# Kernel optimization log

Hardware: AMD Instinct MI355X
Metric: run time of the kernel (lower is better)

Reference implementation:

```python
import jax, jax.numpy as jnp
import numpy as np

EPS = 1e-5


def conv1d(x, w, b):
    # x: (B, C_in, S), w: (C_out, C_in, K), 'same' padding = K//2
    pad = w.shape[-1] // 2
    y = jax.lax.conv_general_dilated(
        x, w, window_strides=(1,), padding=[(pad, pad)],
        dimension_numbers=("NCH", "OIH", "NCH"))
    return y + b[None, :, None]


def layer_norm(x, g, b):
    m = jnp.mean(x, axis=-1, keepdims=True)
    v = jnp.var(x, axis=-1, keepdims=True)
    return (x - m) * jax.lax.rsqrt(v + EPS) * g + b


def duration_predict(x, conv1_w, conv1_b, conv2_w, conv2_b,
                     ln1_g, ln1_b, ln2_g, ln2_b, lin_w, lin_b):
    # x: (B, S, C)
    out = conv1d(jnp.swapaxes(x, -2, -1), conv1_w, conv1_b)          # (B, F, S)
    out = jax.nn.relu(layer_norm(jnp.swapaxes(out, -2, -1), ln1_g, ln1_b))  # (B, S, F)
    out = conv1d(jnp.swapaxes(out, -2, -1), conv2_w, conv2_b)        # (B, F, S)
    out = jax.nn.relu(layer_norm(jnp.swapaxes(out, -2, -1), ln2_g, ln2_b))  # (B, S, F)
    out = jax.nn.relu(out @ lin_w.T + lin_b)                          # (B, S, 1)
    return jnp.squeeze(out, -1)                                       # (B, S)


def setup_inputs() -> dict:
    key = jax.random.key(0)
    ks = jax.random.split(key, 6)
    B, S, C = 16, 1024, 256
    F_, K = 256, 3
    inp = {
        "x": jax.random.normal(ks[0], (B, S, C), dtype=jnp.float32),
        "target": jax.random.uniform(ks[1], (B, S), dtype=jnp.float32),
        "conv1_w": jax.random.normal(ks[2], (F_, C, K), dtype=jnp.float32) * 0.02,
        "conv1_b": jnp.zeros((F_,), dtype=jnp.float32),
        "conv2_w": jax.random.normal(ks[3], (F_, F_, K), dtype=jnp.float32) * 0.02,
        "conv2_b": jnp.zeros((F_,), dtype=jnp.float32),
        "ln1_g": jnp.ones((F_,), dtype=jnp.float32),
        "ln1_b": jnp.zeros((F_,), dtype=jnp.float32),
        "ln2_g": jnp.ones((F_,), dtype=jnp.float32),
        "ln2_b": jnp.zeros((F_,), dtype=jnp.float32),
        "lin_w": jax.random.normal(ks[4], (1, F_), dtype=jnp.float32) * 0.02,
        "lin_b": jnp.zeros((1,), dtype=jnp.float32),
    }
    return inp


def reference(x, target, conv1_w, conv1_b, conv2_w, conv2_b,
              ln1_g, ln1_b, ln2_g, ln2_b, lin_w, lin_b):
    reg_len = duration_predict(x, conv1_w, conv1_b, conv2_w, conv2_b,
                               ln1_g, ln1_b, ln2_g, ln2_b, lin_w, lin_b)
    # Faithful to the original: max_len uses exp(target), the mask uses round(target).
    # max_len is data-dependent -> computed from concrete target (host-side, like the original).
    max_len = int(np.round(float(jnp.max(jnp.sum(jnp.exp(target), axis=-1)))))
    d = jnp.round(target)                 # (B, S) integer-valued durations (banker's rounding, like Python round)
    fin = jnp.cumsum(d, axis=-1)          # (B, S) end offsets
    start = fin - d                       # (B, S) start offsets
    t = jnp.arange(max_len, dtype=target.dtype)  # (T,)
    mask = ((t[None, None, :] >= start[..., None]) &
            (t[None, None, :] < fin[..., None])).astype(x.dtype)  # (B, S, T)
    # x.transpose @ mask -> (B, C, T) -> transpose -> (B, T, C)
    expanded = jnp.einsum("bsc,bst->btc", x, mask)
    return expanded, reg_len
```

## Files before the change

kernel.cpp:

```cpp
#include <hip/hip_runtime.h>
#include <hip/hip_bf16.h>

using frag_ab = __attribute__((ext_vector_type(8))) short;
using frag_cd = __attribute__((ext_vector_type(4))) float;

#define SLEN 1024
#define CDIM 256
#define KTOT 768
#define PD 8

static __device__ __forceinline__ short f2bf(float f) {
    __hip_bfloat16 h = __float2bfloat16(f);
    return *reinterpret_cast<short*>(&h);
}

__global__ __launch_bounds__(1024) void scan_repack_kernel(
    const float* __restrict__ target, int* __restrict__ src, int T,
    const float* __restrict__ w1, __hip_bfloat16* __restrict__ bt1,
    const float* __restrict__ w2, __hip_bfloat16* __restrict__ bt2)
{
    __shared__ int waveSum[16];
    const int tid = threadIdx.x;

    if (blockIdx.x < 16) {
        const int b = blockIdx.x;
        for (int i = tid; i < T; i += 1024) src[b * T + i] = -1;

        const float tv = target[b * SLEN + tid];
        const int d = (int)rintf(tv);

        const int lane = tid & 63;
        const int wid = tid >> 6;
        int v = d;
#pragma unroll
        for (int off = 1; off < 64; off <<= 1) {
            int n = __shfl_up(v, off);
            if (lane >= off) v += n;
        }
        if (lane == 63) waveSum[wid] = v;
        __syncthreads();
        if (tid < 16) {
            int wv = waveSum[tid];
#pragma unroll
            for (int off = 1; off < 16; off <<= 1) {
                int n = __shfl_up(wv, off);
                if (tid >= off) wv += n;
            }
            waveSum[tid] = wv;
        }
        __syncthreads();
        const int fin = v + (wid > 0 ? waveSum[wid - 1] : 0);
        const int start = fin - d;
        for (int t = start; t < fin; ++t)
            if (t >= 0 && t < T) src[b * T + t] = tid;
    } else {
        const int id = (blockIdx.x - 16) * 1024 + tid;
        const int which = id >= 196608;
        const int e = which ? id - 196608 : id;
        const int f = e / KTOT;
        const int K = e - f * KTOT;
        const int k3 = K >> 8;
        const int c = K & 255;
        const float* w = which ? w2 : w1;
        __hip_bfloat16* bt = which ? bt2 : bt1;
        bt[f * KTOT + K] = __float2bfloat16(w[f * KTOT + c * 3 + k3]);
    }
}

__global__ __launch_bounds__(256) void expand_kernel(
    const float* __restrict__ x, const int* __restrict__ src,
    float* __restrict__ out, int T)
{
    const int row = blockIdx.x * 4 + (threadIdx.x >> 6);
    const int lane = threadIdx.x & 63;
    const int nrows = 16 * T;
    if (row >= nrows) return;
    const int b = row / T;
    const int s = src[row];
    float4 val = make_float4(0.f, 0.f, 0.f, 0.f);
    if (s >= 0)
        val = *(const float4*)(x + ((size_t)(b * SLEN + s)) * CDIM + lane * 4);
    *(float4*)(out + (size_t)row * CDIM + lane * 4) = val;
}

__global__ __launch_bounds__(512, 2) void fused_conv(
    const float* __restrict__ x,
    const __hip_bfloat16* __restrict__ bt1,
    const __hip_bfloat16* __restrict__ bt2,
    const float* __restrict__ cb1, const float* __restrict__ g1, const float* __restrict__ be1,
    const float* __restrict__ cb2, const float* __restrict__ g2, const float* __restrict__ be2,
    const float* __restrict__ lw, const float* __restrict__ lb,
    float* __restrict__ reg_len)
{
    __shared__ __align__(16) unsigned char xt[68 * 512];
    __shared__ __align__(16) unsigned char yt[66 * 512];
    __shared__ float red[66][17];
    __shared__ float stats[66][2];

    const int tid = threadIdx.x;
    const int b = blockIdx.y;
    const int s0 = blockIdx.x * 64;

    const int lane = tid & 63;
    const int wid = tid >> 6;
    const int l15 = lane & 15;
    const int lk = lane >> 4;
    const int fbase = wid * 32;

    const __hip_bfloat16* p10 = bt1 + (size_t)(fbase + l15) * KTOT + lk * 8;
    const __hip_bfloat16* p11 = p10 + 16 * KTOT;
    frag_ab pb0[PD], pb1[PD];
#pragma unroll
    for (int i = 0; i < PD; ++i) {
        pb0[i] = *(const frag_ab*)(p10 + i * 32);
        pb1[i] = *(const frag_ab*)(p11 + i * 32);
    }

    const float* xin = x + (size_t)b * SLEN * CDIM;
    for (int ii = tid; ii < 68 * 32; ii += 512) {
        const int r = ii >> 5, cc = ii & 31;
        const int s = s0 - 2 + r;
        frag_ab v = {0, 0, 0, 0, 0, 0, 0, 0};
        if (s >= 0 && s < SLEN) {
            const float4* p = (const float4*)(xin + (size_t)s * CDIM + cc * 8);
            const float4 q0 = p[0], q1 = p[1];
            v[0] = f2bf(q0.x); v[1] = f2bf(q0.y); v[2] = f2bf(q0.z); v[3] = f2bf(q0.w);
            v[4] = f2bf(q1.x); v[5] = f2bf(q1.y); v[6] = f2bf(q1.z); v[7] = f2bf(q1.w);
        }
        *(frag_ab*)(xt + r * 512 + ((cc * 16) ^ ((r & 7) << 4))) = v;
    }
    __syncthreads();

    frag_cd acc1[5][2];
#pragma unroll
    for (int mf = 0; mf < 5; ++mf) {
        acc1[mf][0] = {0.f, 0.f, 0.f, 0.f};
        acc1[mf][1] = {0.f, 0.f, 0.f, 0.f};
    }
#pragma unroll
    for (int kk = 0; kk < 24; ++kk) {
        const frag_ab bb0 = pb0[kk % PD];
        const frag_ab bb1 = pb1[kk % PD];
        if (kk + PD < 24) {
            pb0[kk % PD] = *(const frag_ab*)(p10 + (kk + PD) * 32);
            pb1[kk % PD] = *(const frag_ab*)(p11 + (kk + PD) * 32);
        }
        const int k3 = kk >> 3;
        const int colbyte = (kk & 7) * 64 + lk * 16;
        frag_ab a[5];
#pragma unroll
        for (int mf = 0; mf < 5; ++mf) {
            int r = mf * 16 + l15 + k3;
            if (mf == 4) r = (r > 67) ? 67 : r;
            a[mf] = *(const frag_ab*)(xt + r * 512 + (colbyte ^ ((r & 7) << 4)));
        }
#pragma unroll
        for (int mf = 0; mf < 5; ++mf) {
            acc1[mf][0] = __builtin_amdgcn_mfma_f32_16x16x32_bf16(a[mf], bb0, acc1[mf][0], 0, 0, 0);
            acc1[mf][1] = __builtin_amdgcn_mfma_f32_16x16x32_bf16(a[mf], bb1, acc1[mf][1], 0, 0, 0);
        }
    }

    const __hip_bfloat16* p20 = bt2 + (size_t)(fbase + l15) * KTOT + lk * 8;
    const __hip_bfloat16* p21 = p20 + 16 * KTOT;
    frag_ab qb0[PD], qb1[PD];
#pragma unroll
    for (int i = 0; i < PD; ++i) {
        qb0[i] = *(const frag_ab*)(p20 + i * 32);
        qb1[i] = *(const frag_ab*)(p21 + i * 32);
    }

    {
        const float bias0 = cb1[fbase + l15];
        const float bias1 = cb1[fbase + 16 + l15];
#pragma unroll
        for (int mf = 0; mf < 5; ++mf) {
#pragma unroll
            for (int j = 0; j < 4; ++j) {
                acc1[mf][0][j] += bias0;
                acc1[mf][1][j] += bias1;
                float p = acc1[mf][0][j] + acc1[mf][1][j];
                float q = acc1[mf][0][j] * acc1[mf][0][j] + acc1[mf][1][j] * acc1[mf][1][j];
#pragma unroll
                for (int m = 1; m < 16; m <<= 1) {
                    p += __shfl_xor(p, m);
                    q += __shfl_xor(q, m);
                }
                const bool valid = (mf < 4) || (lk == 0 && j < 2);
                if (l15 == 0 && valid) {
                    const int yr = mf * 16 + lk * 4 + j;
                    red[yr][wid * 2] = p;
                    red[yr][wid * 2 + 1] = q;
                }
            }
        }
    }
    __syncthreads();
    if (tid < 66) {
        float s = 0.f, q = 0.f;
#pragma unroll
        for (int wv = 0; wv < 8; ++wv) { s += red[tid][wv * 2]; q += red[tid][wv * 2 + 1]; }
        const float mean = s * (1.f / 256.f);
        const float var = q * (1.f / 256.f) - mean * mean;
        stats[tid][0] = mean;
        stats[tid][1] = rsqrtf(var + 1e-5f);
    }
    __syncthreads();

    {
        const float ga0 = g1[fbase + l15], ga1 = g1[fbase + 16 + l15];
        const float bb0 = be1[fbase + l15], bb1 = be1[fbase + 16 + l15];
        const int c0b = (fbase + l15) * 2;
        const int c1b = (fbase + 16 + l15) * 2;
#pragma unroll
        for (int mf = 0; mf < 5; ++mf) {
#pragma unroll
            for (int j = 0; j < 4; ++j) {
                const bool valid = (mf < 4) || (lk == 0 && j < 2);
                if (valid) {
                    const int yr = mf * 16 + lk * 4 + j;
                    const float mean = stats[yr][0], rs = stats[yr][1];
                    float v0 = fmaxf((acc1[mf][0][j] - mean) * rs * ga0 + bb0, 0.f);
                    float v1 = fmaxf((acc1[mf][1][j] - mean) * rs * ga1 + bb1, 0.f);
                    const bool zrow = (blockIdx.x == 0 && yr == 0) ||
                                      (blockIdx.x == 15 && yr == 65);
                    if (zrow) { v0 = 0.f; v1 = 0.f; }
                    const int sw = (yr & 7) << 4;
                    *(short*)(yt + yr * 512 + (c0b ^ sw)) = f2bf(v0);
                    *(short*)(yt + yr * 512 + (c1b ^ sw)) = f2bf(v1);
                }
            }
        }
    }
    __syncthreads();

    frag_cd acc2[4][2];
#pragma unroll
    for (int mf = 0; mf < 4; ++mf) {
        acc2[mf][0] = {0.f, 0.f, 0.f, 0.f};
        acc2[mf][1] = {0.f, 0.f, 0.f, 0.f};
    }
#pragma unroll
    for (int kk = 0; kk < 24; ++kk) {
        const frag_ab bb0 = qb0[kk % PD];
        const frag_ab bb1 = qb1[kk % PD];
        if (kk + PD < 24) {
            qb0[kk % PD] = *(const frag_ab*)(p20 + (kk + PD) * 32);
            qb1[kk % PD] = *(const frag_ab*)(p21 + (kk + PD) * 32);
        }
        const int k3 = kk >> 3;
        const int colbyte = (kk & 7) * 64 + lk * 16;
        frag_ab a[4];
#pragma unroll
        for (int mf = 0; mf < 4; ++mf) {
            const int r = mf * 16 + l15 + k3;
            a[mf] = *(const frag_ab*)(yt + r * 512 + (colbyte ^ ((r & 7) << 4)));
        }
#pragma unroll
        for (int mf = 0; mf < 4; ++mf) {
            acc2[mf][0] = __builtin_amdgcn_mfma_f32_16x16x32_bf16(a[mf], bb0, acc2[mf][0], 0, 0, 0);
            acc2[mf][1] = __builtin_amdgcn_mfma_f32_16x16x32_bf16(a[mf], bb1, acc2[mf][1], 0, 0, 0);
        }
    }

    {
        const float bias0 = cb2[fbase + l15];
        const float bias1 = cb2[fbase + 16 + l15];
#pragma unroll
        for (int mf = 0; mf < 4; ++mf) {
#pragma unroll
            for (int j = 0; j < 4; ++j) {
                acc2[mf][0][j] += bias0;
                acc2[mf][1][j] += bias1;
                float p = acc2[mf][0][j] + acc2[mf][1][j];
                float q = acc2[mf][0][j] * acc2[mf][0][j] + acc2[mf][1][j] * acc2[mf][1][j];
#pragma unroll
                for (int m = 1; m < 16; m <<= 1) {
                    p += __shfl_xor(p, m);
                    q += __shfl_xor(q, m);
                }
                if (l15 == 0) {
                    const int row = mf * 16 + lk * 4 + j;
                    red[row][wid * 2] = p;
                    red[row][wid * 2 + 1] = q;
                }
            }
        }
    }
    __syncthreads();
    if (tid < 64) {
        float s = 0.f, q = 0.f;
#pragma unroll
        for (int wv = 0; wv < 8; ++wv) { s += red[tid][wv * 2]; q += red[tid][wv * 2 + 1]; }
        const float mean = s * (1.f / 256.f);
        const float var = q * (1.f / 256.f) - mean * mean;
        stats[tid][0] = mean;
        stats[tid][1] = rsqrtf(var + 1e-5f);
    }
    __syncthreads();

    {
        const float ga0 = g2[fbase + l15], ga1 = g2[fbase + 16 + l15];
        const float bb0 = be2[fbase + l15], bb1 = be2[fbase + 16 + l15];
        const float lw0 = lw[fbase + l15], lw1 = lw[fbase + 16 + l15];
#pragma unroll
        for (int mf = 0; mf < 4; ++mf) {
#pragma unroll
            for (int j = 0; j < 4; ++j) {
                const int row = mf * 16 + lk * 4 + j;
                const float mean = stats[row][0], rs = stats[row][1];
                const float v0 = fmaxf((acc2[mf][0][j] - mean) * rs * ga0 + bb0, 0.f);
                const float v1 = fmaxf((acc2[mf][1][j] - mean) * rs * ga1 + bb1, 0.f);
                float p = v0 * lw0 + v1 * lw1;
#pragma unroll
                for (int m = 1; m < 16; m <<= 1) p += __shfl_xor(p, m);
                if (l15 == 0) red[row][wid * 2] = p;
            }
        }
    }
    __syncthreads();
    if (tid < 64) {
        float s = 0.f;
#pragma unroll
        for (int wv = 0; wv < 8; ++wv) s += red[tid][wv * 2];
        reg_len[b * SLEN + s0 + tid] = fmaxf(s + lb[0], 0.f);
    }
}

extern "C" void kernel_launch(void* const* d_in, const int* in_sizes, int n_in,
                              void* d_out, int out_size, void* d_ws, size_t ws_size,
                              hipStream_t stream)
{
    const float* x       = (const float*)d_in[0];
    const float* target  = (const float*)d_in[1];
    const float* conv1_w = (const float*)d_in[2];
    const float* conv1_b = (const float*)d_in[3];
    const float* conv2_w = (const float*)d_in[4];
    const float* conv2_b = (const float*)d_in[5];
    const float* ln1_g   = (const float*)d_in[6];
    const float* ln1_b   = (const float*)d_in[7];
    const float* ln2_g   = (const float*)d_in[8];
    const float* ln2_b   = (const float*)d_in[9];
    const float* lin_w   = (const float*)d_in[10];
    const float* lin_b   = (const float*)d_in[11];

    const int B = 16, S = 1024, C = 256;
    const int T = (out_size - B * S) / (B * C);

    float* expanded = (float*)d_out;
    float* reg_len  = (float*)d_out + (size_t)B * T * C;

    unsigned char* ws = (unsigned char*)d_ws;
    __hip_bfloat16* bt1 = (__hip_bfloat16*)ws;
    __hip_bfloat16* bt2 = (__hip_bfloat16*)(ws + 393216);
    int* src = (int*)(ws + 2 * 393216);

    scan_repack_kernel<<<400, 1024, 0, stream>>>(
        target, src, T, conv1_w, bt1, conv2_w, bt2);

    fused_conv<<<dim3(16, 16), 512, 0, stream>>>(
        x, bt1, bt2, conv1_b, ln1_g, ln1_b, conv2_b, ln2_g, ln2_b,
        lin_w, lin_b, reg_len);

    expand_kernel<<<(B * T + 3) / 4, 256, 0, stream>>>(x, src, expanded, T);
}
```

Baseline: 54.23 us.

## Merge expand gather into fused conv kernel as extra trailing blocks

```diff
diff --git a/kernel.cpp b/kernel.cpp
--- a/kernel.cpp
+++ b/kernel.cpp
@@ -67,30 +67,15 @@
     }
 }
 
-__global__ __launch_bounds__(256) void expand_kernel(
-    const float* __restrict__ x, const int* __restrict__ src,
-    float* __restrict__ out, int T)
-{
-    const int row = blockIdx.x * 4 + (threadIdx.x >> 6);
-    const int lane = threadIdx.x & 63;
-    const int nrows = 16 * T;
-    if (row >= nrows) return;
-    const int b = row / T;
-    const int s = src[row];
-    float4 val = make_float4(0.f, 0.f, 0.f, 0.f);
-    if (s >= 0)
-        val = *(const float4*)(x + ((size_t)(b * SLEN + s)) * CDIM + lane * 4);
-    *(float4*)(out + (size_t)row * CDIM + lane * 4) = val;
-}
-
-__global__ __launch_bounds__(512, 2) void fused_conv(
+__global__ __launch_bounds__(512, 2) void fused_conv_expand(
     const float* __restrict__ x,
     const __hip_bfloat16* __restrict__ bt1,
     const __hip_bfloat16* __restrict__ bt2,
     const float* __restrict__ cb1, const float* __restrict__ g1, const float* __restrict__ be1,
     const float* __restrict__ cb2, const float* __restrict__ g2, const float* __restrict__ be2,
     const float* __restrict__ lw, const float* __restrict__ lb,
-    float* __restrict__ reg_len)
+    float* __restrict__ reg_len,
+    const int* __restrict__ src, float* __restrict__ expanded, int T)
 {
     __shared__ __align__(16) unsigned char xt[68 * 512];
     __shared__ __align__(16) unsigned char yt[66 * 512];
@@ -98,11 +83,27 @@
     __shared__ float stats[66][2];
 
     const int tid = threadIdx.x;
-    const int b = blockIdx.y;
-    const int s0 = blockIdx.x * 64;
-
     const int lane = tid & 63;
     const int wid = tid >> 6;
+
+    if (blockIdx.x >= 256) {
+        const int row = (blockIdx.x - 256) * 8 + wid;
+        const int nrows = 16 * T;
+        if (row < nrows) {
+            const int b = row / T;
+            const int s = src[row];
+            float4 val = make_float4(0.f, 0.f, 0.f, 0.f);
+            if (s >= 0)
+                val = *(const float4*)(x + ((size_t)(b * SLEN + s)) * CDIM + lane * 4);
+            *(float4*)(expanded + (size_t)row * CDIM + lane * 4) = val;
+        }
+        return;
+    }
+
+    const int b = blockIdx.x >> 4;
+    const int sx = blockIdx.x & 15;
+    const int s0 = sx * 64;
+
     const int l15 = lane & 15;
     const int lk = lane >> 4;
     const int fbase = wid * 32;
@@ -222,8 +223,7 @@
                     const float mean = stats[yr][0], rs = stats[yr][1];
                     float v0 = fmaxf((acc1[mf][0][j] - mean) * rs * ga0 + bb0, 0.f);
                     float v1 = fmaxf((acc1[mf][1][j] - mean) * rs * ga1 + bb1, 0.f);
-                    const bool zrow = (blockIdx.x == 0 && yr == 0) ||
-                                      (blockIdx.x == 15 && yr == 65);
+                    const bool zrow = (sx == 0 && yr == 0) || (sx == 15 && yr == 65);
                     if (zrow) { v0 = 0.f; v1 = 0.f; }
                     const int sw = (yr & 7) << 4;
                     *(short*)(yt + yr * 512 + (c0b ^ sw)) = f2bf(v0);
@@ -358,9 +358,8 @@
     scan_repack_kernel<<<400, 1024, 0, stream>>>(
         target, src, T, conv1_w, bt1, conv2_w, bt2);
 
-    fused_conv<<<dim3(16, 16), 512, 0, stream>>>(
+    const int nExpBlocks = (B * T + 7) / 8;
+    fused_conv_expand<<<256 + nExpBlocks, 512, 0, stream>>>(
         x, bt1, bt2, conv1_b, ln1_g, ln1_b, conv2_b, ln2_g, ln2_b,
-        lin_w, lin_b, reg_len);
-
-    expand_kernel<<<(B * T + 3) / 4, 256, 0, stream>>>(x, src, expanded, T);
+        lin_w, lin_b, reg_len, src, expanded, T);
 }
```

New measurement: 58.75 us. +8.3%, slower.
